# Kernel optimization log

Hardware: AMD Instinct MI355X
Metric: run time of the kernel (lower is better)

Reference implementation:

```python
import jax, jax.numpy as jnp
import numpy as np

B, N, CS, CH, H, K, CT = 16, 256, 256, 64, 8, 32, 1024
NB = 2 * K + 1            # 65 relative-position bins
INF = 1e9
W_L = float(np.sqrt(0.5))
EPS = 1e-5


def setup_inputs() -> dict:
    key = jax.random.key(0)
    ks = jax.random.split(key, 10)
    sc = 0.02
    return {
        "s": jax.random.normal(ks[0], (B, N, CS), jnp.float32),
        "mask": jnp.ones((B, N), dtype=bool),
        "Wq": jax.random.normal(ks[1], (CS, CH * H), jnp.float32) * sc,
        "Wk": jax.random.normal(ks[2], (CS, CH * H), jnp.float32) * sc,
        "Wv": jax.random.normal(ks[3], (CS, CH * H), jnp.float32) * sc,
        "Wb": jax.random.normal(ks[4], (NB, H), jnp.float32) * sc,
        "Wo": jax.random.normal(ks[5], ((NB + CH) * H, CS), jnp.float32) * sc,
        "bo": jnp.zeros((CS,), jnp.float32),
        "ln1_g": jnp.ones((CS,), jnp.float32),
        "ln1_b": jnp.zeros((CS,), jnp.float32),
        "W1": jax.random.normal(ks[6], (CS, CT), jnp.float32) * sc,
        "bf1": jnp.zeros((CT,), jnp.float32),
        "W2": jax.random.normal(ks[7], (CT, CS), jnp.float32) * sc,
        "bf2": jnp.zeros((CS,), jnp.float32),
        "ln2_g": jnp.ones((CS,), jnp.float32),
        "ln2_b": jnp.zeros((CS,), jnp.float32),
    }


def _layernorm(x, g, b):
    m = jnp.mean(x, axis=-1, keepdims=True)
    v = jnp.mean((x - m) ** 2, axis=-1, keepdims=True)
    return (x - m) * jax.lax.rsqrt(v + EPS) * g + b


def reference(s, mask, Wq, Wk, Wv, Wb, Wo, bo, ln1_g, ln1_b, W1, bf1, W2, bf2, ln2_g, ln2_b):
    b_, n = mask.shape
    sq_mask = mask[:, :, None] & mask[:, None, :]            # [B,N,N]
    # one-hot relative position encoding, clipped to [-K, K]
    rel = jnp.clip(jnp.arange(n)[None, :] - jnp.arange(n)[:, None], -K, K) + K
    z = jax.nn.one_hot(rel, NB, dtype=s.dtype)               # [N,N,NB]
    z = z[None] * sq_mask[..., None].astype(s.dtype)         # [B,N,N,NB]

    bias = jnp.einsum('bijn,nh->bhij', z, Wb)                # [B,H,N,N]
    q = (s @ Wq).reshape(b_, n, CH, H).transpose(0, 3, 1, 2)  # [B,H,N,CH]
    k = (s @ Wk).reshape(b_, n, CH, H).transpose(0, 3, 1, 2)
    v = (s @ Wv).reshape(b_, n, CH, H).transpose(0, 3, 1, 2)

    logits = W_L * (jnp.einsum('bhic,bhjc->bhij', q, k) / np.sqrt(CH) + bias)
    logits = logits - INF * (~sq_mask)[:, None, :, :].astype(s.dtype)
    a = jax.nn.softmax(logits, axis=-1)                      # [B,H,N,N]

    o_pair = jnp.einsum('bhij,bijn->bhin', a, z)             # [B,H,N,NB]
    o = jnp.einsum('bhij,bhjc->bhic', a, v)                  # [B,H,N,CH]
    cat = jnp.concatenate([
        o_pair.transpose(0, 2, 1, 3).reshape(b_, n, H * NB),
        o.transpose(0, 2, 1, 3).reshape(b_, n, H * CH),
    ], axis=-1)
    s_upd = cat @ Wo + bo                                    # [B,N,CS]

    s1 = _layernorm(s + s_upd, ln1_g, ln1_b)
    ff = jax.nn.relu(s1 @ W1 + bf1) @ W2 + bf2
    s2 = _layernorm(s1 + ff, ln2_g, ln2_b)
    return (s2, a)
```

## Files before the change

kernel.cpp:

```cpp
#include <hip/hip_runtime.h>
#include <hip/hip_bf16.h>


#define N_TOK 256
#define CH 64
#define NH 8
#define NB 65

typedef __attribute__((ext_vector_type(8))) __bf16 bf16x8;
typedef __attribute__((ext_vector_type(4))) float f32x4;
typedef __attribute__((ext_vector_type(16))) float f32x16;

__device__ inline unsigned short f2bf(float f) {
  unsigned int u = __float_as_uint(f);
  u = (u + 0x7FFFu + ((u >> 16) & 1u)) >> 16;
  return (unsigned short)u;
}
__device__ inline float bf2f(unsigned short u) {
  return __uint_as_float(((unsigned int)u) << 16);
}

__global__ __launch_bounds__(256) void prep_all(
    const float* __restrict__ s, const float* __restrict__ Wq,
    const float* __restrict__ Wk, const float* __restrict__ Wv,
    const float* __restrict__ Wo, const float* __restrict__ W1,
    const float* __restrict__ W2,
    unsigned short* __restrict__ s_bf, unsigned short* __restrict__ wqkv_t,
    unsigned short* __restrict__ wo_t, unsigned short* __restrict__ w1_t,
    unsigned short* __restrict__ w2_t)
{
  const int bid = blockIdx.x, tid = threadIdx.x;
  if (bid < 1024) {
    int idx = (bid * 256 + tid) * 4;
    float4 v = *(const float4*)(s + idx);
    ushort4 o;
    o.x = f2bf(v.x); o.y = f2bf(v.y); o.z = f2bf(v.z); o.w = f2bf(v.w);
    *(ushort4*)(s_bf + idx) = o;
    return;
  }
  int j = bid - 1024;
  const float* in; unsigned short* out;
  int R, C, ldout, r0, c0, qkvperm = 0;
  if (j < 96) {
    int mat = j / 32, jj = j % 32;
    r0 = (jj / 8) * 64; c0 = (jj % 8) * 64;
    in = (mat == 0) ? Wq : (mat == 1) ? Wk : Wv;
    R = 256; C = 512; out = wqkv_t + mat * 131072; ldout = 256; qkvperm = 1;
  } else if (j < 164) {
    int jj = j - 96;
    r0 = (jj / 4) * 64; c0 = (jj % 4) * 64;
    in = Wo; R = 1032; C = 256; out = wo_t; ldout = 1056;
  } else if (j < 228) {
    int jj = j - 164;
    r0 = (jj / 16) * 64; c0 = (jj % 16) * 64;
    in = W1; R = 256; C = 1024; out = w1_t; ldout = 256;
  } else {
    int jj = j - 228;
    r0 = (jj / 4) * 64; c0 = (jj % 4) * 64;
    in = W2; R = 1024; C = 256; out = w2_t; ldout = 1024;
  }
  __shared__ unsigned short lt[64][72];
#pragma unroll
  for (int it = 0; it < 4; ++it) {
    int kk = it * 16 + (tid >> 4);
    int cc = (tid & 15) * 4;
    float4 v = {0.f, 0.f, 0.f, 0.f};
    if (r0 + kk < R) v = *(const float4*)(in + (size_t)(r0 + kk) * C + c0 + cc);
    lt[cc + 0][kk] = f2bf(v.x); lt[cc + 1][kk] = f2bf(v.y);
    lt[cc + 2][kk] = f2bf(v.z); lt[cc + 3][kk] = f2bf(v.w);
  }
  __syncthreads();
  {
    int or_ = tid >> 2, chunk = tid & 3;
    int ocol0 = r0 + chunk * 16;
    int orow = c0 + or_;
    if (qkvperm) orow = (orow & 7) * 64 + (orow >> 3);
    if (ocol0 < ldout) {
      uint4 w0 = *(uint4*)&lt[or_][chunk * 16];
      uint4 w1 = *(uint4*)&lt[or_][chunk * 16 + 8];
      *(uint4*)(out + (size_t)orow * ldout + ocol0) = w0;
      *(uint4*)(out + (size_t)orow * ldout + ocol0 + 8) = w1;
    }
  }
}

__global__ __launch_bounds__(256) void gemm_mfma(
    const unsigned short* __restrict__ A, const unsigned short* __restrict__ Bt,
    int M, int N, int K,
    unsigned short* __restrict__ qk, unsigned short* __restrict__ vt)
{
  __shared__ __align__(16) char Asb[4][8192];
  __shared__ __align__(16) char Bsb[4][8192];
  const int tid = threadIdx.x;
  const int w = tid >> 6, lane = tid & 63;
  const int wm = w >> 1, wn = w & 1;
  const int nbx = gridDim.x;
  int flat = blockIdx.y * nbx + blockIdx.x;
  int cpx = (nbx * gridDim.y) >> 3;
  int swz = (flat & 7) * cpx + (flat >> 3);
  const int m0 = (swz / nbx) * 128, n0 = (swz % nbx) * 128;
  const int fr = lane & 15, kq = lane >> 4;

  const unsigned short *pa[2], *pb[2];
  int ldsoff[2];
#pragma unroll
  for (int s2 = 0; s2 < 2; ++s2) {
    int inst = w * 2 + s2;
    int row = inst * 16 + (lane >> 2);
    int ch = (lane & 3) ^ ((row >> 1) & 3);
    pa[s2] = A + (size_t)(m0 + row) * K + ch * 8;
    pb[s2] = Bt + (size_t)(n0 + row) * K + ch * 8;
    ldsoff[s2] = inst * 1024;
  }
  auto stage = [&](int buf, int koff) {
#pragma unroll
    for (int s2 = 0; s2 < 2; ++s2) {
      __builtin_amdgcn_global_load_lds(
          (const __attribute__((address_space(1))) void*)(pa[s2] + koff),
          (__attribute__((address_space(3))) void*)(Asb[buf] + ldsoff[s2]), 16, 0, 0);
      __builtin_amdgcn_global_load_lds(
          (const __attribute__((address_space(1))) void*)(pb[s2] + koff),
          (__attribute__((address_space(3))) void*)(Bsb[buf] + ldsoff[s2]), 16, 0, 0);
    }
  };

  f32x4 acc[4][4];
#pragma unroll
  for (int m = 0; m < 4; ++m)
#pragma unroll
    for (int n = 0; n < 4; ++n)
#pragma unroll
      for (int e = 0; e < 4; ++e) acc[m][n][e] = 0.f;

  const int nsteps = K >> 5;
  stage(0, 0);
  if (nsteps > 1) stage(1, 32);
  if (nsteps > 2) stage(2, 64);

  for (int t = 0; t < nsteps; ++t) {
    if (t + 3 < nsteps) stage((t + 3) & 3, (t + 3) * 32);
    int ahead = nsteps - 1 - t; if (ahead > 3) ahead = 3;
    switch (ahead) {
      case 3: asm volatile("s_waitcnt vmcnt(12)" ::: "memory"); break;
      case 2: asm volatile("s_waitcnt vmcnt(8)" ::: "memory"); break;
      case 1: asm volatile("s_waitcnt vmcnt(4)" ::: "memory"); break;
      default: asm volatile("s_waitcnt vmcnt(0)" ::: "memory"); break;
    }
    __builtin_amdgcn_s_barrier();

    const char* Ac = Asb[t & 3];
    const char* Bc = Bsb[t & 3];
    bf16x8 af[4], bfr[4];
#pragma unroll
    for (int m = 0; m < 4; ++m) {
      int r = wm * 64 + m * 16 + fr;
      af[m] = *(const bf16x8*)(Ac + r * 64 + ((kq ^ ((r >> 1) & 3)) << 4));
    }
#pragma unroll
    for (int n = 0; n < 4; ++n) {
      int r = wn * 64 + n * 16 + fr;
      bfr[n] = *(const bf16x8*)(Bc + r * 64 + ((kq ^ ((r >> 1) & 3)) << 4));
    }
#pragma unroll
    for (int m = 0; m < 4; ++m)
#pragma unroll
      for (int n = 0; n < 4; ++n)
        acc[m][n] = __builtin_amdgcn_mfma_f32_16x16x32_bf16(af[m], bfr[n], acc[m][n], 0, 0, 0);

    __builtin_amdgcn_s_barrier();
  }

  const int colbase = n0 + wn * 64;
  const int rowbase = m0 + wm * 64 + kq * 4;
#pragma unroll
  for (int mi = 0; mi < 4; ++mi)
#pragma unroll
    for (int ni = 0; ni < 4; ++ni) {
      int col = colbase + ni * 16 + fr;
      int rb = rowbase + mi * 16;
      if (col < 1024) {
#pragma unroll
        for (int r = 0; r < 4; ++r)
          qk[(size_t)(rb + r) * 1024 + col] = f2bf(acc[mi][ni][r]);
      } else {
        int r2 = col & 511;
        int h = r2 >> 6, c = r2 & 63;
        int b = rb >> 8, i = rb & 255;
        union { unsigned short u4[4]; uint2 v; } pk;
#pragma unroll
        for (int r = 0; r < 4; ++r) pk.u4[r] = f2bf(acc[mi][ni][r]);
        *(uint2*)(vt + (((size_t)(b * NH + h)) * CH + c) * N_TOK + i) = pk.v;
      }
    }
}

__global__ __launch_bounds__(256) void gemm_split(
    const unsigned short* __restrict__ A, const unsigned short* __restrict__ Bt,
    int ldk, int koff0, int klen0, int koff1, int klen1,
    unsigned short* __restrict__ CfA, unsigned short* __restrict__ CfB, int ldc)
{
  __shared__ __align__(16) char Asb[4][4096];
  __shared__ __align__(16) char Bsb[4][4096];
  const int tid = threadIdx.x;
  const int w = tid >> 6, lane = tid & 63;
  const int wm = w >> 1, wn = w & 1;
  int flat = (blockIdx.z * gridDim.y + blockIdx.y) * gridDim.x + blockIdx.x;
  int total = gridDim.x * gridDim.y * gridDim.z;
  int swzid = (flat & 7) * (total >> 3) + (flat >> 3);
  const int bx = swzid & 3, by = (swzid >> 2) & 63, z = swzid >> 8;
  const int m0 = by * 64, n0 = bx * 64;
  const int fr = lane & 15, kq = lane >> 4;
  const int koff = z ? koff1 : koff0;
  const int klen = z ? klen1 : klen0;
  unsigned short* Cf = z ? CfB : CfA;

  const int srow = w * 16 + (lane >> 2);
  const int sch = (lane & 3) ^ ((srow >> 1) & 3);
  const unsigned short* pa = A + (size_t)(m0 + srow) * ldk + koff + sch * 8;
  const unsigned short* pb = Bt + (size_t)(n0 + srow) * ldk + koff + sch * 8;

  auto stage = [&](int buf, int ko) {
    __builtin_amdgcn_global_load_lds(
        (const __attribute__((address_space(1))) void*)(pa + ko),
        (__attribute__((address_space(3))) void*)(Asb[buf] + w * 1024), 16, 0, 0);
    __builtin_amdgcn_global_load_lds(
        (const __attribute__((address_space(1))) void*)(pb + ko),
        (__attribute__((address_space(3))) void*)(Bsb[buf] + w * 1024), 16, 0, 0);
  };

  f32x4 acc[2][2];
#pragma unroll
  for (int m = 0; m < 2; ++m)
#pragma unroll
    for (int n = 0; n < 2; ++n)
#pragma unroll
      for (int e = 0; e < 4; ++e) acc[m][n][e] = 0.f;

  const int nsteps = klen >> 5;
  stage(0, 0);
  if (nsteps > 1) stage(1, 32);
  if (nsteps > 2) stage(2, 64);

  for (int t = 0; t < nsteps; ++t) {
    if (t + 3 < nsteps) stage((t + 3) & 3, (t + 3) * 32);
    int ahead = nsteps - 1 - t; if (ahead > 3) ahead = 3;
    switch (ahead) {
      case 3: asm volatile("s_waitcnt vmcnt(6)" ::: "memory"); break;
      case 2: asm volatile("s_waitcnt vmcnt(4)" ::: "memory"); break;
      case 1: asm volatile("s_waitcnt vmcnt(2)" ::: "memory"); break;
      default: asm volatile("s_waitcnt vmcnt(0)" ::: "memory"); break;
    }
    __builtin_amdgcn_s_barrier();

    const char* Ac = Asb[t & 3];
    const char* Bc = Bsb[t & 3];
    bf16x8 af[2], bfr[2];
#pragma unroll
    for (int m = 0; m < 2; ++m) {
      int r = wm * 32 + m * 16 + fr;
      af[m] = *(const bf16x8*)(Ac + r * 64 + ((kq ^ ((r >> 1) & 3)) << 4));
    }
#pragma unroll
    for (int n = 0; n < 2; ++n) {
      int r = wn * 32 + n * 16 + fr;
      bfr[n] = *(const bf16x8*)(Bc + r * 64 + ((kq ^ ((r >> 1) & 3)) << 4));
    }
#pragma unroll
    for (int m = 0; m < 2; ++m)
#pragma unroll
      for (int n = 0; n < 2; ++n)
        acc[m][n] = __builtin_amdgcn_mfma_f32_16x16x32_bf16(af[m], bfr[n], acc[m][n], 0, 0, 0);

    __builtin_amdgcn_s_barrier();
  }

  const int colbase = n0 + wn * 32;
  const int rowbase = m0 + wm * 32 + kq * 4;
#pragma unroll
  for (int mi = 0; mi < 2; ++mi)
#pragma unroll
    for (int ni = 0; ni < 2; ++ni) {
      int col = colbase + ni * 16 + fr;
      int rb = rowbase + mi * 16;
#pragma unroll
      for (int r = 0; r < 4; ++r)
        Cf[(size_t)(rb + r) * ldc + col] = f2bf(acc[mi][ni][r]);
    }
}

__global__ __launch_bounds__(256) void gemm_relu(
    const unsigned short* __restrict__ A, const unsigned short* __restrict__ Bt,
    int N, int K, const float* __restrict__ bias, unsigned short* __restrict__ Cb)
{
  __shared__ __align__(16) char Asb[4][4096];
  __shared__ __align__(16) char Bsb[4][4096];
  const int tid = threadIdx.x;
  const int w = tid >> 6, lane = tid & 63;
  const int wm = w >> 1, wn = w & 1;
  int flat = blockIdx.y * gridDim.x + blockIdx.x;
  int total = gridDim.x * gridDim.y;
  int swzid = (flat & 7) * (total >> 3) + (flat >> 3);
  const int m0 = (swzid / gridDim.x) * 64, n0 = (swzid % gridDim.x) * 64;
  const int fr = lane & 15, kq = lane >> 4;

  const int srow = w * 16 + (lane >> 2);
  const int sch = (lane & 3) ^ ((srow >> 1) & 3);
  const unsigned short* pa = A + (size_t)(m0 + srow) * K + sch * 8;
  const unsigned short* pb = Bt + (size_t)(n0 + srow) * K + sch * 8;

  auto stage = [&](int buf, int koff) {
    __builtin_amdgcn_global_load_lds(
        (const __attribute__((address_space(1))) void*)(pa + koff),
        (__attribute__((address_space(3))) void*)(Asb[buf] + w * 1024), 16, 0, 0);
    __builtin_amdgcn_global_load_lds(
        (const __attribute__((address_space(1))) void*)(pb + koff),
        (__attribute__((address_space(3))) void*)(Bsb[buf] + w * 1024), 16, 0, 0);
  };

  f32x4 acc[2][2];
#pragma unroll
  for (int m = 0; m < 2; ++m)
#pragma unroll
    for (int n = 0; n < 2; ++n)
#pragma unroll
      for (int e = 0; e < 4; ++e) acc[m][n][e] = 0.f;

  const int nsteps = K >> 5;
  stage(0, 0);
  if (nsteps > 1) stage(1, 32);
  if (nsteps > 2) stage(2, 64);

  for (int t = 0; t < nsteps; ++t) {
    if (t + 3 < nsteps) stage((t + 3) & 3, (t + 3) * 32);
    int ahead = nsteps - 1 - t; if (ahead > 3) ahead = 3;
    switch (ahead) {
      case 3: asm volatile("s_waitcnt vmcnt(6)" ::: "memory"); break;
      case 2: asm volatile("s_waitcnt vmcnt(4)" ::: "memory"); break;
      case 1: asm volatile("s_waitcnt vmcnt(2)" ::: "memory"); break;
      default: asm volatile("s_waitcnt vmcnt(0)" ::: "memory"); break;
    }
    __builtin_amdgcn_s_barrier();

    const char* Ac = Asb[t & 3];
    const char* Bc = Bsb[t & 3];
    bf16x8 af[2], bfr[2];
#pragma unroll
    for (int m = 0; m < 2; ++m) {
      int r = wm * 32 + m * 16 + fr;
      af[m] = *(const bf16x8*)(Ac + r * 64 + ((kq ^ ((r >> 1) & 3)) << 4));
    }
#pragma unroll
    for (int n = 0; n < 2; ++n) {
      int r = wn * 32 + n * 16 + fr;
      bfr[n] = *(const bf16x8*)(Bc + r * 64 + ((kq ^ ((r >> 1) & 3)) << 4));
    }
#pragma unroll
    for (int m = 0; m < 2; ++m)
#pragma unroll
      for (int n = 0; n < 2; ++n)
        acc[m][n] = __builtin_amdgcn_mfma_f32_16x16x32_bf16(af[m], bfr[n], acc[m][n], 0, 0, 0);

    __builtin_amdgcn_s_barrier();
  }

  const int colbase = n0 + wn * 32;
  const int rowbase = m0 + wm * 32 + kq * 4;
#pragma unroll
  for (int mi = 0; mi < 2; ++mi)
#pragma unroll
    for (int ni = 0; ni < 2; ++ni) {
      int col = colbase + ni * 16 + fr;
      int rb = rowbase + mi * 16;
      float bv = bias[col];
#pragma unroll
      for (int r = 0; r < 4; ++r)
        Cb[(size_t)(rb + r) * N + col] = f2bf(fmaxf(acc[mi][ni][r] + bv, 0.f));
    }
}

__global__ __launch_bounds__(512, 4) void attn_mfma(
    const unsigned short* __restrict__ qk, const unsigned short* __restrict__ vtg,
    const float* __restrict__ Wb,
    float* __restrict__ a_out, unsigned short* __restrict__ cat)
{
  __shared__ __align__(16) char P_lds[128 * 512];
  __shared__ float wb_lds[65];
  __shared__ float r_lds[128];
  __shared__ float ps_part[2][128], pr_part[2][128], sf_part[2][128];

  const int tid = threadIdx.x;
  const int w = tid >> 6, lane = tid & 63;
  const int iq = w & 3, jh = w >> 2;
  const int bh = blockIdx.y, b = bh >> 3, h = bh & 7;
  const int i0 = blockIdx.x * 128;
  const int l31 = lane & 31, hi = lane >> 5;

  if (tid < 65) wb_lds[tid] = Wb[tid * NH + h];

  if ((bh & 7) == 0) {
    for (int t = tid; t < 128 * 24; t += 512) {
      int r = t / 24, c = t - r * 24;
      cat[((size_t)b * N_TOK + i0 + r) * 1056 + 1032 + c] = 0;
    }
  }

  const int i_loc_l = iq * 32 + l31;
  const int i_glob_l = i0 + i_loc_l;
  const int pswz = i_loc_l & 31;

  const size_t qrow = ((size_t)b * N_TOK + i_glob_l) * 1024 + h * 64;
  bf16x8 qf[4];
#pragma unroll
  for (int ks = 0; ks < 4; ++ks)
    qf[ks] = *(const bf16x8*)(qk + qrow + ks * 16 + hi * 8);

  float psum = 0.f, pre = 0.f, suf = 0.f;
#pragma unroll
  for (int t4 = 0; t4 < 4; ++t4) {
    const int jrow = jh * 128 + t4 * 32 + l31;
    const size_t krow = ((size_t)b * N_TOK + jrow) * 1024 + 512 + h * 64;
    bf16x8 kf[4];
#pragma unroll
    for (int ks = 0; ks < 4; ++ks)
      kf[ks] = *(const bf16x8*)(qk + krow + ks * 16 + hi * 8);
    f32x16 st;
#pragma unroll
    for (int e = 0; e < 16; ++e) st[e] = 0.f;
    __builtin_amdgcn_s_setprio(1);
#pragma unroll
    for (int ks = 0; ks < 4; ++ks)
      st = __builtin_amdgcn_mfma_f32_32x32x16_bf16(kf[ks], qf[ks], st, 0, 0, 0);
    __builtin_amdgcn_s_setprio(0);
#pragma unroll
    for (int q = 0; q < 4; ++q) {
      union { unsigned short u4[4]; uint2 v; } pu;
#pragma unroll
      for (int r = 0; r < 4; ++r) {
        int j = jh * 128 + t4 * 32 + q * 8 + hi * 4 + r;
        int idx = j - i_glob_l + 32;
        idx = idx < 0 ? 0 : (idx > 64 ? 64 : idx);
        float lg = 0.70710678118654752f * (st[q * 4 + r] * 0.125f + wb_lds[idx]);
        float p = __expf(lg);
        psum += p;
        if (j <= i_glob_l - 32) pre += p;
        if (j >= i_glob_l + 32) suf += p;
        pu.u4[r] = f2bf(p);
      }
      int chunk = jh * 16 + t4 * 4 + q;
      *(uint2*)(P_lds + i_loc_l * 512 + ((chunk ^ pswz) << 4) + hi * 8) = pu.v;
    }
  }
  psum += __shfl_xor(psum, 32);
  pre  += __shfl_xor(pre, 32);
  suf  += __shfl_xor(suf, 32);
  if (hi == 0) {
    ps_part[jh][i_loc_l] = psum;
    pr_part[jh][i_loc_l] = pre;
    sf_part[jh][i_loc_l] = suf;
  }
  __syncthreads();
  if (tid < 128) r_lds[tid] = 1.f / (ps_part[0][tid] + ps_part[1][tid]);
  __syncthreads();

  f32x16 oacc;
#pragma unroll
  for (int e = 0; e < 16; ++e) oacc[e] = 0.f;
  const int crow = jh * 32 + l31;
  const unsigned short* vrow = vtg + ((size_t)bh * CH + crow) * N_TOK;
  __builtin_amdgcn_s_setprio(1);
#pragma unroll
  for (int ks = 0; ks < 16; ++ks) {
    bf16x8 pf = *(const bf16x8*)(P_lds + i_loc_l * 512 + (((2 * ks + hi) ^ pswz) << 4));
    bf16x8 vf = *(const bf16x8*)(vrow + ks * 16 + hi * 8);
    oacc = __builtin_amdgcn_mfma_f32_32x32x16_bf16(pf, vf, oacc, 0, 0, 0);
  }
  __builtin_amdgcn_s_setprio(0);
#pragma unroll
  for (int reg = 0; reg < 16; ++reg) {
    int rowp = (reg & 3) + 8 * (reg >> 2) + 4 * hi;
    int i_loc = iq * 32 + rowp;
    float rv = r_lds[i_loc];
    cat[((size_t)b * N_TOK + i0 + i_loc) * 1056 + 520 + h * CH + jh * 32 + l31] =
        f2bf(oacc[reg] * rv);
  }

  for (int rl = 0; rl < 16; ++rl) {
    int i_loc = w * 16 + rl;
    int ig = i0 + i_loc;
    float rv = r_lds[i_loc];
    int j0 = lane * 4;
    ushort4 pv = *(const ushort4*)(P_lds + i_loc * 512 +
        (((lane >> 1) ^ (i_loc & 31)) << 4) + (lane & 1) * 8);
    f32x4 av;
    av[0] = bf2f(pv.x) * rv; av[1] = bf2f(pv.y) * rv;
    av[2] = bf2f(pv.z) * rv; av[3] = bf2f(pv.w) * rv;
    __builtin_nontemporal_store(av,
        (f32x4*)(a_out + ((size_t)bh * N_TOK + ig) * N_TOK + j0));

    unsigned short* crw = cat + ((size_t)b * N_TOK + ig) * 1056 + h * NB;
#pragma unroll
    for (int e = 0; e < 4; ++e) {
      int n = j0 + e - ig + 32;
      if (n >= 1 && n <= 63) crw[n] = f2bf(av[e]);
    }
    if (lane == 0) {
      crw[0]  = f2bf((pr_part[0][i_loc] + pr_part[1][i_loc]) * rv);
      crw[64] = f2bf((sf_part[0][i_loc] + sf_part[1][i_loc]) * rv);
    }
  }
}

__device__ inline float wave_sum(float v) {
#pragma unroll
  for (int off = 32; off; off >>= 1) v += __shfl_xor(v, off);
  return v;
}

__global__ __launch_bounds__(256) void ln_comb2(
    const unsigned short* __restrict__ pA, const unsigned short* __restrict__ pB,
    const float* __restrict__ bias,
    const float* __restrict__ residf, const unsigned short* __restrict__ residb,
    const float* __restrict__ g, const float* __restrict__ bb,
    float* __restrict__ outf, unsigned short* __restrict__ outbf)
{
  const int row = blockIdx.x, tid = threadIdx.x;
  const int wave = tid >> 6, lane = tid & 63;
  size_t idx = (size_t)row * 256 + tid;
  float rv = residf ? residf[idx] : bf2f(residb[idx]);
  float x = bf2f(pA[idx]) + bf2f(pB[idx]) + bias[tid] + rv;
  __shared__ float red[8];
  float s = wave_sum(x);
  if (lane == 0) red[wave] = s;
  __syncthreads();
  float mean = (red[0] + red[1] + red[2] + red[3]) * (1.f / 256.f);
  float d = x - mean;
  float s2 = wave_sum(d * d);
  if (lane == 0) red[4 + wave] = s2;
  __syncthreads();
  float var = (red[4] + red[5] + red[6] + red[7]) * (1.f / 256.f);
  float y = d * rsqrtf(var + 1e-5f) * g[tid] + bb[tid];
  if (outf) outf[idx] = y;
  if (outbf) outbf[idx] = f2bf(y);
}

extern "C" void kernel_launch(void* const* d_in, const int* in_sizes, int n_in,
                              void* d_out, int out_size, void* d_ws, size_t ws_size,
                              hipStream_t stream)
{
  const float* s   = (const float*)d_in[0];
  const float* Wq  = (const float*)d_in[2];
  const float* Wk  = (const float*)d_in[3];
  const float* Wv  = (const float*)d_in[4];
  const float* Wb  = (const float*)d_in[5];
  const float* Wo  = (const float*)d_in[6];
  const float* bo  = (const float*)d_in[7];
  const float* g1  = (const float*)d_in[8];
  const float* b1  = (const float*)d_in[9];
  const float* W1  = (const float*)d_in[10];
  const float* bf1 = (const float*)d_in[11];
  const float* W2  = (const float*)d_in[12];
  const float* bf2 = (const float*)d_in[13];
  const float* g2  = (const float*)d_in[14];
  const float* b2  = (const float*)d_in[15];

  float* out_s2 = (float*)d_out;
  float* a_out  = (float*)d_out + (size_t)16 * 256 * 256;

  char* wsb = (char*)d_ws;
  unsigned short* s_bf   = (unsigned short*)(wsb + 0);
  unsigned short* wqkv_t = (unsigned short*)(wsb + 2097152);
  unsigned short* wo_t   = (unsigned short*)(wsb + 2883584);
  unsigned short* w1_t   = (unsigned short*)(wsb + 3424256);
  unsigned short* w2_t   = (unsigned short*)(wsb + 3948544);
  unsigned short* qk_bf  = (unsigned short*)(wsb + 4718592);
  unsigned short* vt_bf  = (unsigned short*)(wsb + 13107200);
  unsigned short* cat_bf = (unsigned short*)(wsb + 17301504);
  unsigned short* s1_bf  = (unsigned short*)(wsb + 34340864);
  unsigned short* hbuf   = (unsigned short*)(wsb + 36438016);

  unsigned short* woP0 = (unsigned short*)(wsb + 25952256);
  unsigned short* woP1 = (unsigned short*)(wsb + 4718592);
  unsigned short* ffP0 = (unsigned short*)(wsb + 13107200);
  unsigned short* ffP1 = (unsigned short*)(wsb + 8912896);

  dim3 thr(256);

  prep_all<<<1316, thr, 0, stream>>>(s, Wq, Wk, Wv, Wo, W1, W2,
                                     s_bf, wqkv_t, wo_t, w1_t, w2_t);

  gemm_mfma<<<dim3(12, 32), thr, 0, stream>>>(s_bf, wqkv_t, 4096, 1536, 256,
      qk_bf, vt_bf);

  attn_mfma<<<dim3(2, 128), dim3(512), 0, stream>>>(qk_bf, vt_bf, Wb, a_out, cat_bf);

  gemm_split<<<dim3(4, 64, 2), thr, 0, stream>>>(cat_bf, wo_t, 1056,
      0, 544, 544, 512, woP0, woP1, 256);
  ln_comb2<<<4096, thr, 0, stream>>>(woP0, woP1, bo, s, nullptr,
      g1, b1, nullptr, s1_bf);

  gemm_relu<<<dim3(16, 64), thr, 0, stream>>>(s1_bf, w1_t, 1024, 256, bf1, hbuf);

  gemm_split<<<dim3(4, 64, 2), thr, 0, stream>>>(hbuf, w2_t, 1024,
      0, 512, 512, 512, ffP0, ffP1, 256);
  ln_comb2<<<4096, thr, 0, stream>>>(ffP0, ffP1, bf2, nullptr, s1_bf,
      g2, b2, out_s2, nullptr);
}
```

Baseline: 77.22 us.

## Halve attention row tile and split waves between PV MFMA and probability output

The attention kernel now processes 64 query rows per block instead of 128, doubling the grid to 512 blocks and halving LDS use. Within a block, 8 waves split the key dimension four ways for the QK/softmax phase. Afterwards, four waves run the P·V MFMA while the other four write the normalized attention matrix and the pair-feature columns concurrently, where before every wave did both in sequence. This raises block count and occupancy and overlaps the MFMA work with the store-heavy path. In exchange, each block re-reads its K rows for fewer queries and needs a four-way partial-sum reduction.

```diff
diff --git a/kernel.cpp b/kernel.cpp
--- a/kernel.cpp
+++ b/kernel.cpp
@@ -383,22 +383,22 @@
     const float* __restrict__ Wb,
     float* __restrict__ a_out, unsigned short* __restrict__ cat)
 {
-  __shared__ __align__(16) char P_lds[128 * 512];
+  __shared__ __align__(16) char P_lds[64 * 512];
   __shared__ float wb_lds[65];
-  __shared__ float r_lds[128];
-  __shared__ float ps_part[2][128], pr_part[2][128], sf_part[2][128];
+  __shared__ float r_lds[64];
+  __shared__ float ps_part[4][64], pr_part[4][64], sf_part[4][64];
 
   const int tid = threadIdx.x;
   const int w = tid >> 6, lane = tid & 63;
-  const int iq = w & 3, jh = w >> 2;
+  const int iq = w & 1, jq = w >> 1;
   const int bh = blockIdx.y, b = bh >> 3, h = bh & 7;
-  const int i0 = blockIdx.x * 128;
+  const int i0 = blockIdx.x * 64;
   const int l31 = lane & 31, hi = lane >> 5;
 
   if (tid < 65) wb_lds[tid] = Wb[tid * NH + h];
 
   if ((bh & 7) == 0) {
-    for (int t = tid; t < 128 * 24; t += 512) {
+    for (int t = tid; t < 64 * 24; t += 512) {
       int r = t / 24, c = t - r * 24;
       cat[((size_t)b * N_TOK + i0 + r) * 1056 + 1032 + c] = 0;
     }
@@ -416,8 +416,8 @@
 
   float psum = 0.f, pre = 0.f, suf = 0.f;
 #pragma unroll
-  for (int t4 = 0; t4 < 4; ++t4) {
-    const int jrow = jh * 128 + t4 * 32 + l31;
+  for (int t2 = 0; t2 < 2; ++t2) {
+    const int jrow = jq * 64 + t2 * 32 + l31;
     const size_t krow = ((size_t)b * N_TOK + jrow) * 1024 + 512 + h * 64;
     bf16x8 kf[4];
 #pragma unroll
@@ -436,7 +436,7 @@
       union { unsigned short u4[4]; uint2 v; } pu;
 #pragma unroll
       for (int r = 0; r < 4; ++r) {
-        int j = jh * 128 + t4 * 32 + q * 8 + hi * 4 + r;
+        int j = jq * 64 + t2 * 32 + q * 8 + hi * 4 + r;
         int idx = j - i_glob_l + 32;
         idx = idx < 0 ? 0 : (idx > 64 ? 64 : idx);
         float lg = 0.70710678118654752f * (st[q * 4 + r] * 0.125f + wb_lds[idx]);
@@ -446,7 +446,7 @@
         if (j >= i_glob_l + 32) suf += p;
         pu.u4[r] = f2bf(p);
       }
-      int chunk = jh * 16 + t4 * 4 + q;
+      int chunk = jq * 8 + t2 * 4 + q;
       *(uint2*)(P_lds + i_loc_l * 512 + ((chunk ^ pswz) << 4) + hi * 8) = pu.v;
     }
   }
@@ -454,58 +454,70 @@
   pre  += __shfl_xor(pre, 32);
   suf  += __shfl_xor(suf, 32);
   if (hi == 0) {
-    ps_part[jh][i_loc_l] = psum;
-    pr_part[jh][i_loc_l] = pre;
-    sf_part[jh][i_loc_l] = suf;
+    ps_part[jq][i_loc_l] = psum;
+    pr_part[jq][i_loc_l] = pre;
+    sf_part[jq][i_loc_l] = suf;
   }
   __syncthreads();
-  if (tid < 128) r_lds[tid] = 1.f / (ps_part[0][tid] + ps_part[1][tid]);
+  if (tid < 64)
+    r_lds[tid] = 1.f / (ps_part[0][tid] + ps_part[1][tid] +
+                        ps_part[2][tid] + ps_part[3][tid]);
   __syncthreads();
 
-  f32x16 oacc;
-#pragma unroll
-  for (int e = 0; e < 16; ++e) oacc[e] = 0.f;
-  const int crow = jh * 32 + l31;
-  const unsigned short* vrow = vtg + ((size_t)bh * CH + crow) * N_TOK;
-  __builtin_amdgcn_s_setprio(1);
-#pragma unroll
-  for (int ks = 0; ks < 16; ++ks) {
-    bf16x8 pf = *(const bf16x8*)(P_lds + i_loc_l * 512 + (((2 * ks + hi) ^ pswz) << 4));
-    bf16x8 vf = *(const bf16x8*)(vrow + ks * 16 + hi * 8);
-    oacc = __builtin_amdgcn_mfma_f32_32x32x16_bf16(pf, vf, oacc, 0, 0, 0);
-  }
-  __builtin_amdgcn_s_setprio(0);
-#pragma unroll
-  for (int reg = 0; reg < 16; ++reg) {
-    int rowp = (reg & 3) + 8 * (reg >> 2) + 4 * hi;
-    int i_loc = iq * 32 + rowp;
-    float rv = r_lds[i_loc];
-    cat[((size_t)b * N_TOK + i0 + i_loc) * 1056 + 520 + h * CH + jh * 32 + l31] =
-        f2bf(oacc[reg] * rv);
-  }
-
-  for (int rl = 0; rl < 16; ++rl) {
-    int i_loc = w * 16 + rl;
-    int ig = i0 + i_loc;
-    float rv = r_lds[i_loc];
-    int j0 = lane * 4;
-    ushort4 pv = *(const ushort4*)(P_lds + i_loc * 512 +
-        (((lane >> 1) ^ (i_loc & 31)) << 4) + (lane & 1) * 8);
-    f32x4 av;
-    av[0] = bf2f(pv.x) * rv; av[1] = bf2f(pv.y) * rv;
-    av[2] = bf2f(pv.z) * rv; av[3] = bf2f(pv.w) * rv;
-    __builtin_nontemporal_store(av,
-        (f32x4*)(a_out + ((size_t)bh * N_TOK + ig) * N_TOK + j0));
-
-    unsigned short* crw = cat + ((size_t)b * N_TOK + ig) * 1056 + h * NB;
-#pragma unroll
-    for (int e = 0; e < 4; ++e) {
-      int n = j0 + e - ig + 32;
-      if (n >= 1 && n <= 63) crw[n] = f2bf(av[e]);
-    }
-    if (lane == 0) {
-      crw[0]  = f2bf((pr_part[0][i_loc] + pr_part[1][i_loc]) * rv);
-      crw[64] = f2bf((sf_part[0][i_loc] + sf_part[1][i_loc]) * rv);
+  if (w < 4) {
+    const int iq2 = w & 1, ch = w >> 1;
+    const int prow = iq2 * 32 + l31;
+    const int pswz2 = prow & 31;
+    f32x16 oacc;
+#pragma unroll
+    for (int e = 0; e < 16; ++e) oacc[e] = 0.f;
+    const int crow = ch * 32 + l31;
+    const unsigned short* vrow = vtg + ((size_t)bh * CH + crow) * N_TOK;
+    __builtin_amdgcn_s_setprio(1);
+#pragma unroll
+    for (int ks = 0; ks < 16; ++ks) {
+      bf16x8 pf = *(const bf16x8*)(P_lds + prow * 512 + (((2 * ks + hi) ^ pswz2) << 4));
+      bf16x8 vf = *(const bf16x8*)(vrow + ks * 16 + hi * 8);
+      oacc = __builtin_amdgcn_mfma_f32_32x32x16_bf16(pf, vf, oacc, 0, 0, 0);
+    }
+    __builtin_amdgcn_s_setprio(0);
+#pragma unroll
+    for (int reg = 0; reg < 16; ++reg) {
+      int rowp = (reg & 3) + 8 * (reg >> 2) + 4 * hi;
+      int i_loc = iq2 * 32 + rowp;
+      float rv = r_lds[i_loc];
+      cat[((size_t)b * N_TOK + i0 + i_loc) * 1056 + 520 + h * CH + ch * 32 + l31] =
+          f2bf(oacc[reg] * rv);
+    }
+  } else {
+    const int wa = w - 4;
+    for (int rl = 0; rl < 16; ++rl) {
+      int i_loc = wa * 16 + rl;
+      int ig = i0 + i_loc;
+      float rv = r_lds[i_loc];
+      int j0 = lane * 4;
+      ushort4 pv = *(const ushort4*)(P_lds + i_loc * 512 +
+          (((lane >> 1) ^ (i_loc & 31)) << 4) + (lane & 1) * 8);
+      f32x4 av;
+      av[0] = bf2f(pv.x) * rv; av[1] = bf2f(pv.y) * rv;
+      av[2] = bf2f(pv.z) * rv; av[3] = bf2f(pv.w) * rv;
+      __builtin_nontemporal_store(av,
+          (f32x4*)(a_out + ((size_t)bh * N_TOK + ig) * N_TOK + j0));
+
+      unsigned short* crw = cat + ((size_t)b * N_TOK + ig) * 1056 + h * NB;
+#pragma unroll
+      for (int e = 0; e < 4; ++e) {
+        int n = j0 + e - ig + 32;
+        if (n >= 1 && n <= 63) crw[n] = f2bf(av[e]);
+      }
+      if (lane == 0) {
+        float prt = pr_part[0][i_loc] + pr_part[1][i_loc] +
+                    pr_part[2][i_loc] + pr_part[3][i_loc];
+        float sft = sf_part[0][i_loc] + sf_part[1][i_loc] +
+                    sf_part[2][i_loc] + sf_part[3][i_loc];
+        crw[0]  = f2bf(prt * rv);
+        crw[64] = f2bf(sft * rv);
+      }
     }
   }
 }
@@ -591,7 +603,7 @@
   gemm_mfma<<<dim3(12, 32), thr, 0, stream>>>(s_bf, wqkv_t, 4096, 1536, 256,
       qk_bf, vt_bf);
 
-  attn_mfma<<<dim3(2, 128), dim3(512), 0, stream>>>(qk_bf, vt_bf, Wb, a_out, cat_bf);
+  attn_mfma<<<dim3(4, 128), dim3(512), 0, stream>>>(qk_bf, vt_bf, Wb, a_out, cat_bf);
 
   gemm_split<<<dim3(4, 64, 2), thr, 0, stream>>>(cat_bf, wo_t, 1056,
       0, 544, 544, 512, woP0, woP1, 256);
```

New measurement: 77.42 us. Within noise of the previous version (+0.3%).
